# Kernel optimization log

Measured on AMD Instinct MI355X. Metric: run time of the kernel, lower is better.

The kernel has to match this reference:

```python
import jax, jax.numpy as jnp
import numpy as np

N_NODES = 100000


def _gcn_norm(edge_index, num_nodes):
    """Add self-loops and compute symmetric GCN normalization coeffs.
    Returns (row, col, norm) with self-loops appended."""
    loops = jnp.arange(num_nodes, dtype=edge_index.dtype)
    row = jnp.concatenate([edge_index[0], loops])
    col = jnp.concatenate([edge_index[1], loops])
    ones = jnp.ones(row.shape[0], dtype=jnp.float32)
    deg = jax.ops.segment_sum(ones, col, num_segments=num_nodes)
    dinv = jnp.where(deg > 0, jax.lax.rsqrt(deg), 0.0)
    norm = dinv[row] * dinv[col]  # [E + N]
    return row, col, norm


def _gcn_conv(x, W, b, row, col, norm, num_nodes):
    h = x @ W                      # [N, out] dense GEMM first (PyG order)
    msg = h[row] * norm[:, None]   # gather + scale per edge
    agg = jax.ops.segment_sum(msg, col, num_segments=num_nodes)
    return agg + b


def setup_inputs() -> dict:
    key = jax.random.key(0)
    k1, k2, k3, k4 = jax.random.split(key, 4)
    x = jax.random.normal(k1, (N_NODES, 500), dtype=jnp.float32)
    W1 = jax.random.normal(k2, (500, 128), dtype=jnp.float32) * (1.0 / np.sqrt(500))
    b1 = jnp.zeros((128,), dtype=jnp.float32)
    W2 = jax.random.normal(k3, (128, 64), dtype=jnp.float32) * (1.0 / np.sqrt(128))
    b2 = jnp.zeros((64,), dtype=jnp.float32)
    edge_index = jax.random.randint(k4, (2, 3200000), 0, N_NODES, dtype=jnp.int32)
    return {"x": x, "W1": W1, "b1": b1, "W2": W2, "b2": b2,
            "edge_index": edge_index}


def reference(x, W1, b1, W2, b2, edge_index):
    num_nodes = x.shape[0]
    row, col, norm = _gcn_norm(edge_index, num_nodes)
    # encode (dropout is identity in eval mode)
    h = _gcn_conv(x, W1, b1, row, col, norm, num_nodes)
    h = jax.nn.relu(h)
    z = _gcn_conv(h, W2, b2, row, col, norm, num_nodes)
    # decode: per-edge dot product of endpoint embeddings
    scores = jnp.sum(z[edge_index[0]] * z[edge_index[1]], axis=1)  # [E]
    return scores
```

## Files before the change

### kernel.cpp

```cpp
#include <hip/hip_runtime.h>

#define NN 100000
#define K1 500
#define F1 128
#define F2 64

#define NBLK   128
#define BSH    7
#define NBUCK  ((NN + 127) >> 7)
#define NBUCKP 784
#define CAP    6144

typedef __attribute__((ext_vector_type(8))) short short8;
typedef __attribute__((ext_vector_type(4))) float floatx4;

static __device__ __forceinline__ unsigned short f2bf(float f) {
    unsigned int u = __float_as_uint(f);
    unsigned int r = (u + 0x7FFF + ((u >> 16) & 1)) >> 16;
    return (unsigned short)r;
}
static __device__ __forceinline__ void bf2x(unsigned int u, float& lo, float& hi) {
    lo = __uint_as_float(u << 16);
    hi = __uint_as_float(u & 0xffff0000u);
}

__global__ __launch_bounds__(256) void k_pa(const int* __restrict__ col, int E, int chunk,
                                            int* __restrict__ HT) {
    __shared__ int hist[NBUCKP];
    for (int i = threadIdx.x; i < NBUCKP; i += 256) hist[i] = 0;
    __syncthreads();
    const int b = blockIdx.x;
    const int s = b * chunk;
    const int e0 = min(E, s + chunk);
    for (int e = s + threadIdx.x; e < e0; e += 256)
        atomicAdd(&hist[col[e] >> BSH], 1);
    __syncthreads();
    for (int i = threadIdx.x; i < NBUCK; i += 256)
        HT[i * NBLK + b] = hist[i];
}

__global__ __launch_bounds__(128) void k_bsum(const int* __restrict__ HT, int* __restrict__ S) {
    __shared__ int s[128];
    const int tid = threadIdx.x;
    s[tid] = HT[blockIdx.x * NBLK + tid];
    __syncthreads();
    for (int off = 64; off; off >>= 1) {
        if (tid < off) s[tid] += s[tid + off];
        __syncthreads();
    }
    if (tid == 0) S[blockIdx.x] = s[0];
}

__global__ __launch_bounds__(1024) void k_bscan(const int* __restrict__ S,
                                                int* __restrict__ BB, int nb, int E) {
    __shared__ int s[1024];
    const int tid = threadIdx.x;
    int v = (tid < nb) ? S[tid] : 0;
    s[tid] = v;
    __syncthreads();
    for (int off = 1; off < 1024; off <<= 1) {
        int t = (tid >= off) ? s[tid - off] : 0;
        __syncthreads();
        s[tid] += t;
        __syncthreads();
    }
    if (tid < nb) BB[tid] = s[tid] - v;
    if (tid == 0) BB[nb] = E;
}

__global__ __launch_bounds__(128) void k_boff(int* __restrict__ HT, const int* __restrict__ BB) {
    __shared__ int s[128];
    const int tid = threadIdx.x;
    const int rowb = blockIdx.x * NBLK;
    int v = HT[rowb + tid];
    s[tid] = v;
    __syncthreads();
    for (int off = 1; off < 128; off <<= 1) {
        int t = (tid >= off) ? s[tid - off] : 0;
        __syncthreads();
        s[tid] += t;
        __syncthreads();
    }
    HT[rowb + tid] = s[tid] - v + BB[blockIdx.x];
}

__global__ __launch_bounds__(256) void k_pc(const int* __restrict__ row,
                                            const int* __restrict__ col, int E, int chunk,
                                            const int* __restrict__ HT,
                                            unsigned long long* __restrict__ pairs) {
    __shared__ int cur[NBUCKP];
    const int b = blockIdx.x;
    for (int i = threadIdx.x; i < NBUCK; i += 256) cur[i] = HT[i * NBLK + b];
    __syncthreads();
    const int s = b * chunk;
    const int e0 = min(E, s + chunk);
    for (int e = s + threadIdx.x; e < e0; e += 256) {
        const int r = row[e], c = col[e];
        const int p = atomicAdd(&cur[c >> BSH], 1);
        pairs[p] = ((unsigned long long)(unsigned)c << 32) | (unsigned)r;
    }
}

__global__ __launch_bounds__(256) void k_pd(const unsigned long long* __restrict__ pairs,
                                            const int* __restrict__ BB,
                                            int* __restrict__ ptr, float* __restrict__ dinv,
                                            int* __restrict__ idx) {
    __shared__ int colcnt[128], colptr[128], cur[128];
    __shared__ int lidx[CAP];
    const int buck = blockIdx.x;
    const int base = BB[buck];
    int count = BB[buck + 1] - base;
    if (count > CAP) count = CAP;
    const int lo = buck << BSH;
    const int tid = threadIdx.x;
    if (tid < 128) colcnt[tid] = 0;
    __syncthreads();
    for (int e = tid; e < count; e += 256) {
        const int c = (int)(pairs[base + e] >> 32);
        atomicAdd(&colcnt[c & 127], 1);
    }
    __syncthreads();
    if (tid < 128) colptr[tid] = colcnt[tid];
    __syncthreads();
    for (int off = 1; off < 128; off <<= 1) {
        int t = 0;
        if (tid < 128 && tid >= off) t = colptr[tid - off];
        __syncthreads();
        if (tid < 128) colptr[tid] += t;
        __syncthreads();
    }
    if (tid < 128) {
        const int excl = colptr[tid] - colcnt[tid];
        cur[tid] = excl;
        const int c = lo + tid;
        if (c < NN) {
            ptr[c]  = base + excl;
            dinv[c] = rsqrtf((float)colcnt[tid] + 1.0f);
        }
    }
    __syncthreads();
    for (int e = tid; e < count; e += 256) {
        const unsigned long long pr = pairs[base + e];
        const int c = (int)(pr >> 32);
        const int p = atomicAdd(&cur[c & 127], 1);
        lidx[p] = (int)(pr & 0xffffffffu);
    }
    __syncthreads();
    for (int e = tid; e < count; e += 256)
        idx[base + e] = lidx[e];
}

__global__ __launch_bounds__(256) void k_w1t(const float* __restrict__ W1,
                                             unsigned short* __restrict__ W1T) {
    int t = blockIdx.x * 256 + threadIdx.x;
    int n = t >> 9, k = t & 511;
    W1T[t] = (k < K1) ? f2bf(W1[k * F1 + n]) : (unsigned short)0;
}

__global__ __launch_bounds__(256) void k_gemm1_mfma(
    const float* __restrict__ x,
    const unsigned short* __restrict__ W1T,
    const float* __restrict__ dinv,
    unsigned short* __restrict__ h)
{
    const int wave = threadIdx.x >> 6;
    const int lane = threadIdx.x & 63;
    const int q    = lane >> 4;
    const int m16  = lane & 15;
    const int rowBase = blockIdx.x * 128 + wave * 32;

    floatx4 acc[2][8];
#pragma unroll
    for (int a = 0; a < 2; ++a)
#pragma unroll
        for (int b = 0; b < 8; ++b) acc[a][b] = (floatx4){0.f, 0.f, 0.f, 0.f};

    int row0 = rowBase + m16;      if (row0 > NN - 1) row0 = NN - 1;
    int row1 = rowBase + 16 + m16; if (row1 > NN - 1) row1 = NN - 1;
    const size_t rb[2] = {(size_t)row0 * K1, (size_t)row1 * K1};

#pragma unroll 3
    for (int k0 = 0; k0 < 480; k0 += 32) {
        const int kk = k0 + q * 8;
        short8 afr[2], bfr[8];
#pragma unroll
        for (int mt = 0; mt < 2; ++mt) {
            const floatx4 v0 = *(const floatx4*)(x + rb[mt] + kk);
            const floatx4 v1 = *(const floatx4*)(x + rb[mt] + kk + 4);
            short8 t;
            t[0] = f2bf(v0[0]); t[1] = f2bf(v0[1]); t[2] = f2bf(v0[2]); t[3] = f2bf(v0[3]);
            t[4] = f2bf(v1[0]); t[5] = f2bf(v1[1]); t[6] = f2bf(v1[2]); t[7] = f2bf(v1[3]);
            afr[mt] = t;
        }
#pragma unroll
        for (int nt = 0; nt < 8; ++nt)
            bfr[nt] = *(const short8*)(W1T + (nt * 16 + m16) * 512 + kk);
#pragma unroll
        for (int mt = 0; mt < 2; ++mt)
#pragma unroll
            for (int nt = 0; nt < 8; ++nt)
                acc[mt][nt] = __builtin_amdgcn_mfma_f32_16x16x32_bf16(
                    afr[mt], bfr[nt], acc[mt][nt], 0, 0, 0);
    }
    {
        const int kk = 480 + q * 8;
        short8 afr[2], bfr[8];
#pragma unroll
        for (int mt = 0; mt < 2; ++mt) {
            short8 t;
#pragma unroll
            for (int j = 0; j < 8; ++j) {
                const int k = kk + j;
                t[j] = (k < K1) ? (short)f2bf(x[rb[mt] + k]) : (short)0;
            }
            afr[mt] = t;
        }
#pragma unroll
        for (int nt = 0; nt < 8; ++nt)
            bfr[nt] = *(const short8*)(W1T + (nt * 16 + m16) * 512 + kk);
#pragma unroll
        for (int mt = 0; mt < 2; ++mt)
#pragma unroll
            for (int nt = 0; nt < 8; ++nt)
                acc[mt][nt] = __builtin_amdgcn_mfma_f32_16x16x32_bf16(
                    afr[mt], bfr[nt], acc[mt][nt], 0, 0, 0);
    }
#pragma unroll
    for (int mt = 0; mt < 2; ++mt) {
        const int rbase = rowBase + mt * 16 + q * 4;
#pragma unroll
        for (int r = 0; r < 4; ++r) {
            const int row = rbase + r;
            if (row < NN) {
                const float dr = dinv[row];
#pragma unroll
                for (int nt = 0; nt < 8; ++nt)
                    h[(size_t)row * F1 + nt * 16 + m16] = f2bf(acc[mt][nt][r] * dr);
            }
        }
    }
}

__global__ __launch_bounds__(256) void k_agg1(const int* __restrict__ ptr,
                                              const int* __restrict__ idx, int E,
                                              const float* __restrict__ dinv,
                                              const unsigned short* __restrict__ h,
                                              float* __restrict__ agg) {
    const int c    = blockIdx.x * 4 + (threadIdx.x >> 6);
    const int lane = threadIdx.x & 63;
    const int es = lane >> 3, fg = lane & 7;
    float acc[16];
#pragma unroll
    for (int j = 0; j < 16; ++j) acc[j] = 0.f;
    if (es == 0) {
        const uint4 u0 = *(const uint4*)(h + (size_t)c * F1 + fg * 16);
        const uint4 u1 = *(const uint4*)(h + (size_t)c * F1 + fg * 16 + 8);
        bf2x(u0.x, acc[0], acc[1]);  bf2x(u0.y, acc[2], acc[3]);
        bf2x(u0.z, acc[4], acc[5]);  bf2x(u0.w, acc[6], acc[7]);
        bf2x(u1.x, acc[8], acc[9]);  bf2x(u1.y, acc[10], acc[11]);
        bf2x(u1.z, acc[12], acc[13]); bf2x(u1.w, acc[14], acc[15]);
    }
    const int s   = ptr[c];
    const int end = (c + 1 < NN) ? ptr[c + 1] : E;
    int e = s + es;
    for (; e + 8 < end; e += 16) {
        const int r0 = idx[e], r1 = idx[e + 8];
        const uint4 u00 = *(const uint4*)(h + (size_t)r0 * F1 + fg * 16);
        const uint4 u01 = *(const uint4*)(h + (size_t)r0 * F1 + fg * 16 + 8);
        const uint4 u10 = *(const uint4*)(h + (size_t)r1 * F1 + fg * 16);
        const uint4 u11 = *(const uint4*)(h + (size_t)r1 * F1 + fg * 16 + 8);
        float lo, hi;
        bf2x(u00.x, lo, hi); acc[0] += lo; acc[1] += hi;
        bf2x(u00.y, lo, hi); acc[2] += lo; acc[3] += hi;
        bf2x(u00.z, lo, hi); acc[4] += lo; acc[5] += hi;
        bf2x(u00.w, lo, hi); acc[6] += lo; acc[7] += hi;
        bf2x(u01.x, lo, hi); acc[8] += lo; acc[9] += hi;
        bf2x(u01.y, lo, hi); acc[10] += lo; acc[11] += hi;
        bf2x(u01.z, lo, hi); acc[12] += lo; acc[13] += hi;
        bf2x(u01.w, lo, hi); acc[14] += lo; acc[15] += hi;
        bf2x(u10.x, lo, hi); acc[0] += lo; acc[1] += hi;
        bf2x(u10.y, lo, hi); acc[2] += lo; acc[3] += hi;
        bf2x(u10.z, lo, hi); acc[4] += lo; acc[5] += hi;
        bf2x(u10.w, lo, hi); acc[6] += lo; acc[7] += hi;
        bf2x(u11.x, lo, hi); acc[8] += lo; acc[9] += hi;
        bf2x(u11.y, lo, hi); acc[10] += lo; acc[11] += hi;
        bf2x(u11.z, lo, hi); acc[12] += lo; acc[13] += hi;
        bf2x(u11.w, lo, hi); acc[14] += lo; acc[15] += hi;
    }
    if (e < end) {
        const int r = idx[e];
        const uint4 u0 = *(const uint4*)(h + (size_t)r * F1 + fg * 16);
        const uint4 u1 = *(const uint4*)(h + (size_t)r * F1 + fg * 16 + 8);
        float lo, hi;
        bf2x(u0.x, lo, hi); acc[0] += lo; acc[1] += hi;
        bf2x(u0.y, lo, hi); acc[2] += lo; acc[3] += hi;
        bf2x(u0.z, lo, hi); acc[4] += lo; acc[5] += hi;
        bf2x(u0.w, lo, hi); acc[6] += lo; acc[7] += hi;
        bf2x(u1.x, lo, hi); acc[8] += lo; acc[9] += hi;
        bf2x(u1.y, lo, hi); acc[10] += lo; acc[11] += hi;
        bf2x(u1.z, lo, hi); acc[12] += lo; acc[13] += hi;
        bf2x(u1.w, lo, hi); acc[14] += lo; acc[15] += hi;
    }
#pragma unroll
    for (int j = 0; j < 16; ++j) {
        acc[j] += __shfl_xor(acc[j], 8);
        acc[j] += __shfl_xor(acc[j], 16);
        acc[j] += __shfl_xor(acc[j], 32);
    }
    if (es == 0) {
        const float dc = dinv[c];
        float* o = agg + (size_t)c * F1 + fg * 16;
        float4 o0 = {acc[0] * dc, acc[1] * dc, acc[2] * dc, acc[3] * dc};
        float4 o1 = {acc[4] * dc, acc[5] * dc, acc[6] * dc, acc[7] * dc};
        float4 o2 = {acc[8] * dc, acc[9] * dc, acc[10] * dc, acc[11] * dc};
        float4 o3 = {acc[12] * dc, acc[13] * dc, acc[14] * dc, acc[15] * dc};
        *(float4*)(o)      = o0;
        *(float4*)(o + 4)  = o1;
        *(float4*)(o + 8)  = o2;
        *(float4*)(o + 12) = o3;
    }
}

__global__ __launch_bounds__(256) void k_gemm2(const float* __restrict__ agg1,
                                               const float* __restrict__ b1,
                                               const float* __restrict__ W2,
                                               const float* __restrict__ dinv,
                                               unsigned short* __restrict__ h2) {
    __shared__ __align__(16) float W2s[F1 * F2];
    __shared__ __align__(16) float xs[64 * F1];
    const int tid = threadIdx.x;
    const int r0  = blockIdx.x * 64;
    for (int i = tid; i < F1 * F2; i += 256) W2s[i] = W2[i];
    const int base = r0 * F1;
    for (int i = tid; i < 64 * F1; i += 256) {
        int gi = base + i;
        float v = 0.f;
        if (gi < NN * F1) v = fmaxf(agg1[gi] + b1[i & (F1 - 1)], 0.f);
        xs[i] = v;
    }
    __syncthreads();

    const int j = tid & 63;
    const int g = tid >> 6;
    float acc[16];
#pragma unroll
    for (int rr = 0; rr < 16; ++rr) acc[rr] = 0.f;

    for (int k = 0; k < F1; k += 4) {
        const float w0 = W2s[(k + 0) * F2 + j];
        const float w1 = W2s[(k + 1) * F2 + j];
        const float w2 = W2s[(k + 2) * F2 + j];
        const float w3 = W2s[(k + 3) * F2 + j];
#pragma unroll
        for (int rr = 0; rr < 16; ++rr) {
            const float4 xv = *(const float4*)&xs[(g * 16 + rr) * F1 + k];
            acc[rr] += xv.x * w0 + xv.y * w1 + xv.z * w2 + xv.w * w3;
        }
    }
#pragma unroll
    for (int rr = 0; rr < 16; ++rr) {
        int r = r0 + g * 16 + rr;
        if (r < NN) h2[(size_t)r * F2 + j] = f2bf(acc[rr] * dinv[r]);
    }
}

__global__ __launch_bounds__(256) void k_agg2(const int* __restrict__ ptr,
                                              const int* __restrict__ idx, int E,
                                              const float* __restrict__ dinv,
                                              const unsigned short* __restrict__ h2,
                                              const float* __restrict__ b2,
                                              unsigned short* __restrict__ z) {
    const int c    = blockIdx.x * 4 + (threadIdx.x >> 6);
    const int lane = threadIdx.x & 63;
    const int es = lane >> 3, fg = lane & 7;
    float a[8];
#pragma unroll
    for (int j = 0; j < 8; ++j) a[j] = 0.f;
    if (es == 0) {
        const uint4 u = *(const uint4*)(h2 + (size_t)c * F2 + fg * 8);
        bf2x(u.x, a[0], a[1]); bf2x(u.y, a[2], a[3]);
        bf2x(u.z, a[4], a[5]); bf2x(u.w, a[6], a[7]);
    }
    const int s   = ptr[c];
    const int end = (c + 1 < NN) ? ptr[c + 1] : E;
    int e = s + es;
    for (; e + 8 < end; e += 16) {
        const int r0 = idx[e], r1 = idx[e + 8];
        const uint4 u0 = *(const uint4*)(h2 + (size_t)r0 * F2 + fg * 8);
        const uint4 u1 = *(const uint4*)(h2 + (size_t)r1 * F2 + fg * 8);
        float lo, hi;
        bf2x(u0.x, lo, hi); a[0] += lo; a[1] += hi;
        bf2x(u0.y, lo, hi); a[2] += lo; a[3] += hi;
        bf2x(u0.z, lo, hi); a[4] += lo; a[5] += hi;
        bf2x(u0.w, lo, hi); a[6] += lo; a[7] += hi;
        bf2x(u1.x, lo, hi); a[0] += lo; a[1] += hi;
        bf2x(u1.y, lo, hi); a[2] += lo; a[3] += hi;
        bf2x(u1.z, lo, hi); a[4] += lo; a[5] += hi;
        bf2x(u1.w, lo, hi); a[6] += lo; a[7] += hi;
    }
    if (e < end) {
        const int r = idx[e];
        const uint4 u = *(const uint4*)(h2 + (size_t)r * F2 + fg * 8);
        float lo, hi;
        bf2x(u.x, lo, hi); a[0] += lo; a[1] += hi;
        bf2x(u.y, lo, hi); a[2] += lo; a[3] += hi;
        bf2x(u.z, lo, hi); a[4] += lo; a[5] += hi;
        bf2x(u.w, lo, hi); a[6] += lo; a[7] += hi;
    }
#pragma unroll
    for (int j = 0; j < 8; ++j) {
        a[j] += __shfl_xor(a[j], 8);
        a[j] += __shfl_xor(a[j], 16);
        a[j] += __shfl_xor(a[j], 32);
    }
    if (es == 0) {
        const float dc = dinv[c];
        const float4 b0 = *(const float4*)(b2 + fg * 8);
        const float4 b1v = *(const float4*)(b2 + fg * 8 + 4);
        uint4 o;
        o.x = (unsigned)f2bf(a[0] * dc + b0.x)  | ((unsigned)f2bf(a[1] * dc + b0.y)  << 16);
        o.y = (unsigned)f2bf(a[2] * dc + b0.z)  | ((unsigned)f2bf(a[3] * dc + b0.w)  << 16);
        o.z = (unsigned)f2bf(a[4] * dc + b1v.x) | ((unsigned)f2bf(a[5] * dc + b1v.y) << 16);
        o.w = (unsigned)f2bf(a[6] * dc + b1v.z) | ((unsigned)f2bf(a[7] * dc + b1v.w) << 16);
        *(uint4*)(z + (size_t)c * F2 + fg * 8) = o;
    }
}

__global__ void k_decode(const int* __restrict__ src, const int* __restrict__ dst,
                         int E, const unsigned short* __restrict__ z,
                         float* __restrict__ out) {
    long t = (long)blockIdx.x * blockDim.x + threadIdx.x;
    int e = (int)(t >> 3);
    int l = (int)(t & 7);
    if (e >= E) return;
    const int s = src[e], d = dst[e];
    const uint4 us = *(const uint4*)(z + (size_t)s * F2 + l * 8);
    const uint4 ud = *(const uint4*)(z + (size_t)d * F2 + l * 8);
    float sl, sh, dl, dh;
    float v;
    bf2x(us.x, sl, sh); bf2x(ud.x, dl, dh); v  = sl * dl + sh * dh;
    bf2x(us.y, sl, sh); bf2x(ud.y, dl, dh); v += sl * dl + sh * dh;
    bf2x(us.z, sl, sh); bf2x(ud.z, dl, dh); v += sl * dl + sh * dh;
    bf2x(us.w, sl, sh); bf2x(ud.w, dl, dh); v += sl * dl + sh * dh;
    v += __shfl_down(v, 4, 8);
    v += __shfl_down(v, 2, 8);
    v += __shfl_down(v, 1, 8);
    if (l == 0) out[e] = v;
}

extern "C" void kernel_launch(void* const* d_in, const int* in_sizes, int n_in,
                              void* d_out, int out_size, void* d_ws, size_t ws_size,
                              hipStream_t stream) {
    const float* x  = (const float*)d_in[0];
    const float* W1 = (const float*)d_in[1];
    const float* b1 = (const float*)d_in[2];
    const float* W2 = (const float*)d_in[3];
    const float* b2 = (const float*)d_in[4];
    const int*   ei = (const int*)d_in[5];
    const int E = in_sizes[5] / 2;
    const int* rowp = ei;
    const int* colp = ei + E;

    char* wsb = (char*)d_ws;
    float* dinv = (float*)wsb;                 wsb += 100352 * 4;
    int*   ptr  = (int*)wsb;                   wsb += 100352 * 4;
    int*   S    = (int*)wsb;                   wsb += 1024 * 4;
    int*   BB   = (int*)wsb;                   wsb += 1024 * 4;
    int*   HT   = (int*)wsb;                   wsb += (size_t)1024 * NBLK * 4;
    int*   idx  = (int*)wsb;                   wsb += (size_t)E * 4;
    unsigned short* W1T = (unsigned short*)wsb; wsb += 128 * 512 * 2;
    unsigned short* hbf = (unsigned short*)wsb; wsb += (size_t)NN * F1 * 2;
    float* agg1 = (float*)wsb;                 wsb += (size_t)NN * F1 * 4;
    unsigned short* h2 = (unsigned short*)wsb; wsb += (size_t)NN * F2 * 2;
    unsigned long long* pairs = (unsigned long long*)agg1;
    unsigned short* z = hbf;
    float* out  = (float*)d_out;

    const int chunk = (E + NBLK - 1) / NBLK;

    k_pa   <<<NBLK, 256, 0, stream>>>(colp, E, chunk, HT);
    k_bsum <<<NBUCK, 128, 0, stream>>>(HT, S);
    k_bscan<<<1, 1024, 0, stream>>>(S, BB, NBUCK, E);
    k_boff <<<NBUCK, 128, 0, stream>>>(HT, BB);
    k_pc   <<<NBLK, 256, 0, stream>>>(rowp, colp, E, chunk, HT, pairs);
    k_pd   <<<NBUCK, 256, 0, stream>>>(pairs, BB, ptr, dinv, idx);

    k_w1t<<<256, 256, 0, stream>>>(W1, W1T);
    k_gemm1_mfma<<<(NN + 127) / 128, 256, 0, stream>>>(x, W1T, dinv, hbf);
    k_agg1<<<NN / 4, 256, 0, stream>>>(ptr, idx, E, dinv, hbf, agg1);

    k_gemm2<<<(NN + 63) / 64, 256, 0, stream>>>(agg1, b1, W2, dinv, h2);
    k_agg2<<<NN / 4, 256, 0, stream>>>(ptr, idx, E, dinv, h2, b2, z);

    const long dthreads = (long)E * 8;
    k_decode<<<(int)((dthreads + 255) / 256), 256, 0, stream>>>(
        rowp, colp, E, z, out);
}
```

Before: 833.9 us.

## Double-buffer x tiles in LDS via async global_load_lds and packed bf16 convert

The first-layer GEMM kernel now stages 128x32 fp32 tiles of x into a swizzled, double-buffered LDS buffer using global_load_lds. The next tile's load is issued before the current tile is computed. Fragments are read from LDS and converted with the hardware packed bf16 instruction instead of manual rounding. The aim is to hide global latency and cut conversion ALU work. In exchange it adds LDS use and a block-wide barrier every k-step, which may reduce occupancy.

```diff
diff --git a/kernel.cpp b/kernel.cpp
--- a/kernel.cpp
+++ b/kernel.cpp
@@ -13,6 +13,7 @@
 
 typedef __attribute__((ext_vector_type(8))) short short8;
 typedef __attribute__((ext_vector_type(4))) float floatx4;
+typedef __attribute__((ext_vector_type(4))) unsigned int uintx4;
 
 static __device__ __forceinline__ unsigned short f2bf(float f) {
     unsigned int u = __float_as_uint(f);
@@ -22,6 +23,17 @@
 static __device__ __forceinline__ void bf2x(unsigned int u, float& lo, float& hi) {
     lo = __uint_as_float(u << 16);
     hi = __uint_as_float(u & 0xffff0000u);
+}
+static __device__ __forceinline__ unsigned int cvtpk(float lo, float hi) {
+    unsigned int r;
+    asm("v_cvt_pk_bf16_f32 %0, %1, %2" : "=v"(r) : "v"(lo), "v"(hi));
+    return r;
+}
+
+typedef __attribute__((address_space(3))) unsigned int u32_lds;
+typedef const __attribute__((address_space(1))) unsigned int u32_g;
+static __device__ __forceinline__ void stage16(const float* g, float* l) {
+    __builtin_amdgcn_global_load_lds((u32_g*)g, (u32_lds*)l, 16, 0, 0);
 }
 
 __global__ __launch_bounds__(256) void k_pa(const int* __restrict__ col, int E, int chunk,
@@ -163,11 +175,17 @@
     const float* __restrict__ dinv,
     unsigned short* __restrict__ h)
 {
-    const int wave = threadIdx.x >> 6;
-    const int lane = threadIdx.x & 63;
+    __shared__ __align__(16) float xbuf[2 * 128 * 32];
+    const int tid  = threadIdx.x;
+    const int wave = tid >> 6;
+    const int lane = tid & 63;
     const int q    = lane >> 4;
     const int m16  = lane & 15;
-    const int rowBase = blockIdx.x * 128 + wave * 32;
+    const int blkRow  = blockIdx.x * 128;
+    const int rowBase = blkRow + wave * 32;
+
+    const int sr = tid >> 3;
+    const int sc = tid & 7;
 
     floatx4 acc[2][8];
 #pragma unroll
@@ -179,18 +197,48 @@
     int row1 = rowBase + 16 + m16; if (row1 > NN - 1) row1 = NN - 1;
     const size_t rb[2] = {(size_t)row0 * K1, (size_t)row1 * K1};
 
-#pragma unroll 3
-    for (int k0 = 0; k0 < 480; k0 += 32) {
+    const int lr[2] = {wave * 32 + m16, wave * 32 + 16 + m16};
+
+    {
+#pragma unroll
+        for (int i = 0; i < 4; ++i) {
+            const int r  = i * 32 + sr;
+            int gr = blkRow + r; if (gr > NN - 1) gr = NN - 1;
+            const float* src = x + (size_t)gr * K1 + ((sc ^ (r & 7)) << 2);
+            stage16(src, xbuf + (size_t)(i * 256 + tid) * 4);
+        }
+    }
+    __syncthreads();
+
+    for (int t = 0; t < 15; ++t) {
+        const int k0 = t * 32;
+        if (t < 14) {
+            float* dbase = xbuf + ((t + 1) & 1) * 4096;
+#pragma unroll
+            for (int i = 0; i < 4; ++i) {
+                const int r  = i * 32 + sr;
+                int gr = blkRow + r; if (gr > NN - 1) gr = NN - 1;
+                const float* src = x + (size_t)gr * K1 + (k0 + 32) + ((sc ^ (r & 7)) << 2);
+                stage16(src, dbase + (size_t)(i * 256 + tid) * 4);
+            }
+        }
+        const float* buf = xbuf + (t & 1) * 4096;
         const int kk = k0 + q * 8;
+
         short8 afr[2], bfr[8];
 #pragma unroll
         for (int mt = 0; mt < 2; ++mt) {
-            const floatx4 v0 = *(const floatx4*)(x + rb[mt] + kk);
-            const floatx4 v1 = *(const floatx4*)(x + rb[mt] + kk + 4);
-            short8 t;
-            t[0] = f2bf(v0[0]); t[1] = f2bf(v0[1]); t[2] = f2bf(v0[2]); t[3] = f2bf(v0[3]);
-            t[4] = f2bf(v1[0]); t[5] = f2bf(v1[1]); t[6] = f2bf(v1[2]); t[7] = f2bf(v1[3]);
-            afr[mt] = t;
+            const int r  = lr[mt];
+            const int c0 = (2 * q)     ^ (r & 7);
+            const int c1 = (2 * q + 1) ^ (r & 7);
+            const floatx4 v0 = *(const floatx4*)(buf + r * 32 + c0 * 4);
+            const floatx4 v1 = *(const floatx4*)(buf + r * 32 + c1 * 4);
+            uintx4 p;
+            p[0] = cvtpk(v0[0], v0[1]);
+            p[1] = cvtpk(v0[2], v0[3]);
+            p[2] = cvtpk(v1[0], v1[1]);
+            p[3] = cvtpk(v1[2], v1[3]);
+            afr[mt] = __builtin_bit_cast(short8, p);
         }
 #pragma unroll
         for (int nt = 0; nt < 8; ++nt)
@@ -201,6 +249,7 @@
             for (int nt = 0; nt < 8; ++nt)
                 acc[mt][nt] = __builtin_amdgcn_mfma_f32_16x16x32_bf16(
                     afr[mt], bfr[nt], acc[mt][nt], 0, 0, 0);
+        __syncthreads();
     }
     {
         const int kk = 480 + q * 8;
```

After: 823.3 us. Within noise of the previous version (-1.3%).

## Stage x tiles into swizzled LDS and hold W1 fragments in registers

Applied to the files above, without the earlier changes.

The first GEMM is rebuilt. Each block now covers 32 rows, and each wave owns 32 output columns with its W1 bf16 fragments held in registers for the whole K range. The x tile is brought into XOR-swizzled shared memory with direct global-to-LDS loads, then converted with packed bf16 instructions. This removes the redundant per-wave W1 loads and the uncoalesced direct x reads. In exchange it uses 64KB of LDS per block, which limits occupancy, and it has no overlap between the staging phase and the MFMA phase.

```diff
diff --git a/kernel.cpp b/kernel.cpp
--- a/kernel.cpp
+++ b/kernel.cpp
@@ -13,6 +13,7 @@
 
 typedef __attribute__((ext_vector_type(8))) short short8;
 typedef __attribute__((ext_vector_type(4))) float floatx4;
+typedef __attribute__((ext_vector_type(4))) unsigned int uintx4;
 
 static __device__ __forceinline__ unsigned short f2bf(float f) {
     unsigned int u = __float_as_uint(f);
@@ -22,6 +23,17 @@
 static __device__ __forceinline__ void bf2x(unsigned int u, float& lo, float& hi) {
     lo = __uint_as_float(u << 16);
     hi = __uint_as_float(u & 0xffff0000u);
+}
+static __device__ __forceinline__ unsigned int cvtpk(float lo, float hi) {
+    unsigned int r;
+    asm("v_cvt_pk_bf16_f32 %0, %1, %2" : "=v"(r) : "v"(lo), "v"(hi));
+    return r;
+}
+
+typedef __attribute__((address_space(3))) unsigned int u32_lds;
+typedef const __attribute__((address_space(1))) unsigned int u32_g;
+static __device__ __forceinline__ void stage16(const float* g, float* l) {
+    __builtin_amdgcn_global_load_lds((u32_g*)g, (u32_lds*)l, 16, 0, 0);
 }
 
 __global__ __launch_bounds__(256) void k_pa(const int* __restrict__ col, int E, int chunk,
@@ -157,86 +169,81 @@
     W1T[t] = (k < K1) ? f2bf(W1[k * F1 + n]) : (unsigned short)0;
 }
 
-__global__ __launch_bounds__(256) void k_gemm1_mfma(
+__global__ __launch_bounds__(256, 2) void k_gemm1_mfma(
     const float* __restrict__ x,
     const unsigned short* __restrict__ W1T,
     const float* __restrict__ dinv,
     unsigned short* __restrict__ h)
 {
-    const int wave = threadIdx.x >> 6;
-    const int lane = threadIdx.x & 63;
+    __shared__ __align__(16) float xs[32 * 512];
+    const int tid  = threadIdx.x;
+    const int wave = tid >> 6;
+    const int lane = tid & 63;
     const int q    = lane >> 4;
     const int m16  = lane & 15;
-    const int rowBase = blockIdx.x * 128 + wave * 32;
-
-    floatx4 acc[2][8];
-#pragma unroll
-    for (int a = 0; a < 2; ++a)
-#pragma unroll
-        for (int b = 0; b < 8; ++b) acc[a][b] = (floatx4){0.f, 0.f, 0.f, 0.f};
-
-    int row0 = rowBase + m16;      if (row0 > NN - 1) row0 = NN - 1;
-    int row1 = rowBase + 16 + m16; if (row1 > NN - 1) row1 = NN - 1;
-    const size_t rb[2] = {(size_t)row0 * K1, (size_t)row1 * K1};
-
-#pragma unroll 3
-    for (int k0 = 0; k0 < 480; k0 += 32) {
-        const int kk = k0 + q * 8;
-        short8 afr[2], bfr[8];
+    const int blkRow  = blockIdx.x * 32;
+    const int colBase = wave * 32;
+
+    short8 bw[2][16];
+#pragma unroll
+    for (int nt = 0; nt < 2; ++nt)
+#pragma unroll
+        for (int t = 0; t < 16; ++t)
+            bw[nt][t] = *(const short8*)(W1T + (colBase + nt * 16 + m16) * 512 + t * 32 + q * 8);
+
+#pragma unroll
+    for (int i = 0; i < 16; ++i) {
+        const int s = i * 256 + tid;
+        const int r = s >> 7;
+        const int c = s & 127;
+        int cs = c ^ (r & 7);
+        if (cs > 124) cs = 124;
+        const float* src = x + (size_t)(blkRow + r) * K1 + cs * 4;
+        stage16(src, xs + (size_t)s * 4);
+    }
+    __syncthreads();
+
+    floatx4 acc[2][2];
+#pragma unroll
+    for (int mt = 0; mt < 2; ++mt)
+#pragma unroll
+        for (int nt = 0; nt < 2; ++nt) acc[mt][nt] = (floatx4){0.f, 0.f, 0.f, 0.f};
+
+#pragma unroll
+    for (int t = 0; t < 16; ++t) {
+        short8 afr[2];
 #pragma unroll
         for (int mt = 0; mt < 2; ++mt) {
-            const floatx4 v0 = *(const floatx4*)(x + rb[mt] + kk);
-            const floatx4 v1 = *(const floatx4*)(x + rb[mt] + kk + 4);
-            short8 t;
-            t[0] = f2bf(v0[0]); t[1] = f2bf(v0[1]); t[2] = f2bf(v0[2]); t[3] = f2bf(v0[3]);
-            t[4] = f2bf(v1[0]); t[5] = f2bf(v1[1]); t[6] = f2bf(v1[2]); t[7] = f2bf(v1[3]);
-            afr[mt] = t;
+            const int rr = mt * 16 + m16;
+            const int c0 = t * 8 + (( 2 * q )     ^ (rr & 7));
+            const int c1 = t * 8 + (( 2 * q + 1 ) ^ (rr & 7));
+            const floatx4 v0 = *(const floatx4*)(xs + rr * 512 + c0 * 4);
+            const floatx4 v1 = *(const floatx4*)(xs + rr * 512 + c1 * 4);
+            uintx4 p;
+            p[0] = cvtpk(v0[0], v0[1]);
+            p[1] = cvtpk(v0[2], v0[3]);
+            p[2] = cvtpk(v1[0], v1[1]);
+            p[3] = cvtpk(v1[2], v1[3]);
+            afr[mt] = __builtin_bit_cast(short8, p);
         }
 #pragma unroll
-        for (int nt = 0; nt < 8; ++nt)
-            bfr[nt] = *(const short8*)(W1T + (nt * 16 + m16) * 512 + kk);
-#pragma unroll
         for (int mt = 0; mt < 2; ++mt)
 #pragma unroll
-            for (int nt = 0; nt < 8; ++nt)
+            for (int nt = 0; nt < 2; ++nt)
                 acc[mt][nt] = __builtin_amdgcn_mfma_f32_16x16x32_bf16(
-                    afr[mt], bfr[nt], acc[mt][nt], 0, 0, 0);
-    }
-    {
-        const int kk = 480 + q * 8;
-        short8 afr[2], bfr[8];
-#pragma unroll
-        for (int mt = 0; mt < 2; ++mt) {
-            short8 t;
-#pragma unroll
-            for (int j = 0; j < 8; ++j) {
-                const int k = kk + j;
-                t[j] = (k < K1) ? (short)f2bf(x[rb[mt] + k]) : (short)0;
-            }
-            afr[mt] = t;
-        }
-#pragma unroll
-        for (int nt = 0; nt < 8; ++nt)
-            bfr[nt] = *(const short8*)(W1T + (nt * 16 + m16) * 512 + kk);
-#pragma unroll
-        for (int mt = 0; mt < 2; ++mt)
-#pragma unroll
-            for (int nt = 0; nt < 8; ++nt)
-                acc[mt][nt] = __builtin_amdgcn_mfma_f32_16x16x32_bf16(
-                    afr[mt], bfr[nt], acc[mt][nt], 0, 0, 0);
-    }
+                    afr[mt], bw[nt][t], acc[mt][nt], 0, 0, 0);
+    }
+
 #pragma unroll
     for (int mt = 0; mt < 2; ++mt) {
-        const int rbase = rowBase + mt * 16 + q * 4;
+        const int rbase = blkRow + mt * 16 + q * 4;
 #pragma unroll
         for (int r = 0; r < 4; ++r) {
             const int row = rbase + r;
-            if (row < NN) {
-                const float dr = dinv[row];
-#pragma unroll
-                for (int nt = 0; nt < 8; ++nt)
-                    h[(size_t)row * F1 + nt * 16 + m16] = f2bf(acc[mt][nt][r] * dr);
-            }
+            const float dr = dinv[row];
+#pragma unroll
+            for (int nt = 0; nt < 2; ++nt)
+                h[(size_t)row * F1 + colBase + nt * 16 + m16] = f2bf(acc[mt][nt][r] * dr);
         }
     }
 }
@@ -486,7 +493,7 @@
     k_pd   <<<NBUCK, 256, 0, stream>>>(pairs, BB, ptr, dinv, idx);
 
     k_w1t<<<256, 256, 0, stream>>>(W1, W1T);
-    k_gemm1_mfma<<<(NN + 127) / 128, 256, 0, stream>>>(x, W1T, dinv, hbf);
+    k_gemm1_mfma<<<NN / 32, 256, 0, stream>>>(x, W1T, dinv, hbf);
     k_agg1<<<NN / 4, 256, 0, stream>>>(ptr, idx, E, dinv, hbf, agg1);
 
     k_gemm2<<<(NN + 63) / 64, 256, 0, stream>>>(agg1, b1, W2, dinv, h2);
```

New measurement: 790.9 us. -5.1%, faster.
